# Kernel tuning notes

Hardware: AMD Instinct MI355X
Metric: run time of the kernel (lower is better)

The kernel has to match this reference:

```python
import jax, jax.numpy as jnp
import numpy as np

POSITIVE_MULT = 3.0  # init kwarg positive_mult
MIN_K = 10


def _ohem_single(pred, tgt):
    """OHEM MSE for one flattened sample. pred, tgt: [N]."""
    N = pred.shape[0]
    loss = (pred - tgt) ** 2  # elementwise MSE (reduction='none')
    pos = tgt > 0
    num_pos = jnp.sum(pos.astype(jnp.int32))
    # k = num_pos * positive_mult, clamped so k + num_pos <= N  =>  k = min(3p, N-p)
    k = jnp.minimum((num_pos.astype(jnp.float32) * POSITIVE_MULT).astype(jnp.int32),
                    N - num_pos)
    full_mean = jnp.mean(loss)
    # positive mean (safe denom; branch unused when num_pos small => k < 10)
    pos_mean = jnp.sum(jnp.where(pos, loss, 0.0)) / jnp.maximum(num_pos, 1).astype(loss.dtype)
    # top-k over negative losses: mask positives to -inf, sort descending,
    # take first k via index mask (k is traced, so no dynamic shapes)
    neg_loss = jnp.where(pos, -jnp.inf, loss)
    sorted_desc = -jnp.sort(-neg_loss)
    idx = jnp.arange(N)
    topk_mean = jnp.sum(jnp.where(idx < k, sorted_desc, 0.0)) / jnp.maximum(k, 1).astype(loss.dtype)
    ohem = pos_mean + topk_mean
    return jnp.where(k < MIN_K, full_mean, ohem)


def reference(x, char_target, aff_target):
    B, _, H, W = x.shape
    pred_r = x[:, 0].reshape(B, -1)  # region scores
    pred_a = x[:, 1].reshape(B, -1)  # affinity scores
    # bilinear resize, half-pixel centers == torch align_corners=False
    ct = jax.image.resize(char_target, (B, 1, H, W), method='bilinear').reshape(B, -1)
    at = jax.image.resize(aff_target, (B, 1, H, W), method='bilinear').reshape(B, -1)
    char_loss = jax.vmap(_ohem_single)(pred_r, ct)  # [B]
    aff_loss = jax.vmap(_ohem_single)(pred_a, at)   # [B]
    return jnp.mean(char_loss + aff_loss)


def setup_inputs() -> dict:
    key = jax.random.key(0)
    k1, k2, k3 = jax.random.split(key, 3)
    x = jax.random.normal(k1, (32, 2, 640, 640), dtype=jnp.float32)
    char_target = jax.random.normal(k2, (32, 1, 320, 320), dtype=jnp.float32)
    aff_target = jax.random.normal(k3, (32, 1, 320, 320), dtype=jnp.float32)
    return {"x": x, "char_target": char_target, "aff_target": aff_target}
```

## Files before the change

### kernel.cpp

```cpp
#include <hip/hip_runtime.h>

#define NS 64
#define HH 640
#define WW 640
#define NPIX (HH * WW)
#define TH 320
#define TW 320
#define MINK 10
#define BPS 40
#define TPB 320
#define ITERS 4

__device__ __forceinline__ float resize_scalar(const float* __restrict__ tgt, int y, int xc) {
    float sy = fmaxf(0.5f * (float)y - 0.25f, 0.0f);
    int y0 = (int)sy;
    float fy = sy - (float)y0;
    int y1 = min(y0 + 1, TH - 1);
    float sx = fmaxf(0.5f * (float)xc - 0.25f, 0.0f);
    int x0 = (int)sx;
    float fx = sx - (float)x0;
    int x1 = min(x0 + 1, TW - 1);
    const float* r0 = tgt + y0 * TW;
    const float* r1 = tgt + y1 * TW;
    float top = (1.0f - fx) * r0[x0] + fx * r0[x1];
    float bot = (1.0f - fx) * r1[x0] + fx * r1[x1];
    return (1.0f - fy) * top + fy * bot;
}

__global__ __launch_bounds__(TPB) void k_reduce(const float* __restrict__ x,
                                                const float* __restrict__ ct,
                                                const float* __restrict__ at,
                                                float* __restrict__ partA,
                                                float* __restrict__ partP,
                                                int* __restrict__ partC) {
    int bid = blockIdx.x;
    int s = bid / BPS, blk = bid % BPS;
    int b = s >> 1, c = s & 1;
    const float* pred = x + (size_t)s * NPIX;
    const float* tgt = (c == 0 ? ct : at) + (size_t)b * (TH * TW);

    int tid = threadIdx.x;
    int u = tid % 80;
    int rr = tid / 80;
    int rbase = blk * 16;

    float fy = (rr & 1) ? 0.25f : 0.75f;
    float gy = 1.0f - fy;
    int xq = 4 * u;
    int xl = max(xq - 1, 0);
    int xr = min(xq + 4, TW - 1);

    float sA = 0.0f, sP = 0.0f;
    int cP = 0;

#pragma unroll
    for (int i = 0; i < ITERS; ++i) {
        int y = rbase + rr + 4 * i;
        int y0raw = (y >> 1) + (y & 1) - 1;
        int y0 = max(y0raw, 0);
        int y1 = min(y0raw + 1, TH - 1);
        const float* r0 = tgt + y0 * TW;
        const float* r1 = tgt + y1 * TW;

        float4 a4 = *reinterpret_cast<const float4*>(r0 + xq);
        float La = r0[xl], Ra = r0[xr];
        float4 b4 = *reinterpret_cast<const float4*>(r1 + xq);
        float Lb = r1[xl], Rb = r1[xr];

        float mL = gy * La + fy * Lb;
        float m0 = gy * a4.x + fy * b4.x;
        float m1 = gy * a4.y + fy * b4.y;
        float m2 = gy * a4.z + fy * b4.z;
        float m3 = gy * a4.w + fy * b4.w;
        float mR = gy * Ra + fy * Rb;

        float tv[8];
        tv[0] = 0.25f * mL + 0.75f * m0;
        tv[1] = 0.75f * m0 + 0.25f * m1;
        tv[2] = 0.25f * m0 + 0.75f * m1;
        tv[3] = 0.75f * m1 + 0.25f * m2;
        tv[4] = 0.25f * m1 + 0.75f * m2;
        tv[5] = 0.75f * m2 + 0.25f * m3;
        tv[6] = 0.25f * m2 + 0.75f * m3;
        tv[7] = 0.75f * m3 + 0.25f * mR;

        const float* pr = pred + y * WW + 8 * u;
        float4 p0 = *reinterpret_cast<const float4*>(pr);
        float4 p1 = *reinterpret_cast<const float4*>(pr + 4);
        float pv[8] = {p0.x, p0.y, p0.z, p0.w, p1.x, p1.y, p1.z, p1.w};

#pragma unroll
        for (int j = 0; j < 8; ++j) {
            float d = pv[j] - tv[j];
            float l = d * d;
            sA += l;
            bool pos = tv[j] > 0.0f;
            sP += pos ? l : 0.0f;
            cP += pos ? 1 : 0;
        }
    }

    for (int off = 32; off > 0; off >>= 1) {
        sA += __shfl_down(sA, off);
        sP += __shfl_down(sP, off);
        cP += __shfl_down(cP, off);
    }
    __shared__ float shA[5], shP[5];
    __shared__ int shC[5];
    int w = tid >> 6;
    if ((tid & 63) == 0) { shA[w] = sA; shP[w] = sP; shC[w] = cP; }
    __syncthreads();
    if (tid == 0) {
        float a = 0.0f, p = 0.0f;
        int ci = 0;
        for (int q = 0; q < 5; ++q) { a += shA[q]; p += shP[q]; ci += shC[q]; }
        partA[s * BPS + blk] = a;
        partP[s * BPS + blk] = p;
        partC[s * BPS + blk] = ci;
    }
}

__global__ __launch_bounds__(256) void k_topk(const float* __restrict__ x,
                                              const float* __restrict__ ct,
                                              const float* __restrict__ at,
                                              const int* __restrict__ partC,
                                              float* __restrict__ topk) {
    int s = blockIdx.x;
    __shared__ int pSh;
    if (threadIdx.x < 64) {
        int v = (threadIdx.x < BPS) ? partC[s * BPS + threadIdx.x] : 0;
        for (int off = 32; off > 0; off >>= 1) v += __shfl_down(v, off);
        if (threadIdx.x == 0) pSh = v;
    }
    __syncthreads();
    int p = pSh;
    int k = min((int)((float)p * 3.0f), NPIX - p);
    if (k < MINK || k >= NPIX - p) return;

    int b = s >> 1, c = s & 1;
    const float* pred = x + (size_t)s * NPIX;
    const float* tgt = (c == 0 ? ct : at) + (size_t)b * (TH * TW);

    __shared__ unsigned int hcnt[2048];
    __shared__ float hsum[2048];
    __shared__ unsigned int selBin;
    __shared__ unsigned int remShared;
    __shared__ float sumTopShared;

    if (threadIdx.x == 0) { remShared = (unsigned int)k; sumTopShared = 0.0f; }

    const int shiftv[3] = {21, 10, 0};
    const unsigned int maskv[3] = {0x7FFu, 0x7FFu, 0x3FFu};
    unsigned int prefix = 0;

    for (int pass = 0; pass < 3; ++pass) {
        for (int i = threadIdx.x; i < 2048; i += 256) { hcnt[i] = 0u; hsum[i] = 0.0f; }
        __syncthreads();
        for (int e = threadIdx.x; e < NPIX; e += 256) {
            int yy = e / WW, xx = e % WW;
            float tv = resize_scalar(tgt, yy, xx);
            if (tv > 0.0f) continue;
            float d = pred[e] - tv;
            float l = d * d;
            unsigned int bits = __float_as_uint(l);
            bool match;
            if (pass == 0) match = true;
            else if (pass == 1) match = ((bits >> 21) == prefix);
            else match = ((bits >> 10) == prefix);
            if (match) {
                unsigned int bin = (bits >> shiftv[pass]) & maskv[pass];
                atomicAdd(&hcnt[bin], 1u);
                atomicAdd(&hsum[bin], l);
            }
        }
        __syncthreads();
        if (threadIdx.x == 0) {
            unsigned int remS = remShared;
            int nb = (int)maskv[pass] + 1;
            unsigned int cum = 0; float sAbove = 0.0f; unsigned int bsel = 0;
            for (int bin = nb - 1; bin >= 0; --bin) {
                unsigned int cc = hcnt[bin];
                if (cum + cc >= remS) { bsel = (unsigned int)bin; break; }
                cum += cc; sAbove += hsum[bin];
            }
            selBin = bsel;
            remShared = remS - cum;
            sumTopShared += sAbove;
        }
        __syncthreads();
        if (pass == 0) prefix = selBin;
        else if (pass == 1) prefix = (prefix << 11) | selBin;
        __syncthreads();
    }
    if (threadIdx.x == 0) {
        unsigned int bits = (prefix << 10) | selBin;
        float v = __uint_as_float(bits);
        topk[s] = sumTopShared + (float)remShared * v;
    }
}

__global__ void k_final(const float* __restrict__ partA, const float* __restrict__ partP,
                        const int* __restrict__ partC, const float* __restrict__ topk,
                        float* __restrict__ out) {
    int s = threadIdx.x;
    float a = 0.0f, pp = 0.0f;
    int p = 0;
    const float4* pa4 = reinterpret_cast<const float4*>(partA + s * BPS);
    const float4* pp4 = reinterpret_cast<const float4*>(partP + s * BPS);
    const int4*   pc4 = reinterpret_cast<const int4*>(partC + s * BPS);
#pragma unroll
    for (int q = 0; q < BPS / 4; ++q) {
        float4 va = pa4[q]; a += va.x + va.y + va.z + va.w;
        float4 vp = pp4[q]; pp += vp.x + vp.y + vp.z + vp.w;
        int4 vc = pc4[q]; p += vc.x + vc.y + vc.z + vc.w;
    }
    int k = min((int)((float)p * 3.0f), NPIX - p);
    float lossv;
    if (k < MINK) {
        lossv = a / (float)NPIX;
    } else {
        float nn = a - pp;
        float tsum = (k >= NPIX - p) ? nn : topk[s];
        lossv = pp / (float)max(p, 1) + tsum / (float)max(k, 1);
    }
    for (int off = 32; off > 0; off >>= 1) lossv += __shfl_down(lossv, off);
    if (s == 0) out[0] = lossv / 32.0f;
}

extern "C" void kernel_launch(void* const* d_in, const int* in_sizes, int n_in,
                              void* d_out, int out_size, void* d_ws, size_t ws_size,
                              hipStream_t stream) {
    const float* x  = (const float*)d_in[0];
    const float* ct = (const float*)d_in[1];
    const float* at = (const float*)d_in[2];
    float* out = (float*)d_out;

    float* partA = (float*)d_ws;
    float* partP = partA + NS * BPS;
    int*   partC = (int*)(partP + NS * BPS);
    float* topk  = (float*)(partC + NS * BPS);

    k_reduce<<<dim3(NS * BPS), dim3(TPB), 0, stream>>>(x, ct, at, partA, partP, partC);
    k_topk<<<dim3(NS), dim3(256), 0, stream>>>(x, ct, at, partC, topk);
    k_final<<<dim3(1), dim3(64), 0, stream>>>(partA, partP, partC, topk, out);
}
```

Measured before the change: 30.84 us.

## Fuse reduce, top-k and final kernels via last-block completion counters

Merges the three kernels into one launch: each block writes its partial sums, bumps a per-sample and then a global atomic counter, and the last block to finish performs the final combine and any needed top-k radix selection serially over samples. It also remaps block indices across 8 groups and transposes the partial-sum layout. This removes inter-kernel launch gaps and the separate top-k and final launches, at the cost of a memset and of running any top-k selection on a single workgroup, which would be slow if that path were ever taken.

```diff
diff --git a/kernel.cpp b/kernel.cpp
--- a/kernel.cpp
+++ b/kernel.cpp
@@ -10,6 +10,7 @@
 #define BPS 40
 #define TPB 320
 #define ITERS 4
+#define NWG (NS * BPS)
 
 __device__ __forceinline__ float resize_scalar(const float* __restrict__ tgt, int y, int xc) {
     float sy = fmaxf(0.5f * (float)y - 0.25f, 0.0f);
@@ -27,13 +28,17 @@
     return (1.0f - fy) * top + fy * bot;
 }
 
-__global__ __launch_bounds__(TPB) void k_reduce(const float* __restrict__ x,
-                                                const float* __restrict__ ct,
-                                                const float* __restrict__ at,
-                                                float* __restrict__ partA,
-                                                float* __restrict__ partP,
-                                                int* __restrict__ partC) {
-    int bid = blockIdx.x;
+__global__ __launch_bounds__(TPB) void k_fused(const float* __restrict__ x,
+                                               const float* __restrict__ ct,
+                                               const float* __restrict__ at,
+                                               float* __restrict__ partA,
+                                               float* __restrict__ partP,
+                                               int* __restrict__ partC,
+                                               int* __restrict__ cntS,
+                                               int* __restrict__ cntG,
+                                               float* __restrict__ out) {
+    int orig = blockIdx.x;
+    int bid = (orig & 7) * (NWG >> 3) + (orig >> 3);
     int s = bid / BPS, blk = bid % BPS;
     int b = s >> 1, c = s & 1;
     const float* pred = x + (size_t)s * NPIX;
@@ -110,121 +115,125 @@
     int w = tid >> 6;
     if ((tid & 63) == 0) { shA[w] = sA; shP[w] = sP; shC[w] = cP; }
     __syncthreads();
+
+    __shared__ int lastFlag;
     if (tid == 0) {
         float a = 0.0f, p = 0.0f;
         int ci = 0;
         for (int q = 0; q < 5; ++q) { a += shA[q]; p += shP[q]; ci += shC[q]; }
-        partA[s * BPS + blk] = a;
-        partP[s * BPS + blk] = p;
-        partC[s * BPS + blk] = ci;
-    }
-}
-
-__global__ __launch_bounds__(256) void k_topk(const float* __restrict__ x,
-                                              const float* __restrict__ ct,
-                                              const float* __restrict__ at,
-                                              const int* __restrict__ partC,
-                                              float* __restrict__ topk) {
-    int s = blockIdx.x;
-    __shared__ int pSh;
-    if (threadIdx.x < 64) {
-        int v = (threadIdx.x < BPS) ? partC[s * BPS + threadIdx.x] : 0;
-        for (int off = 32; off > 0; off >>= 1) v += __shfl_down(v, off);
-        if (threadIdx.x == 0) pSh = v;
-    }
-    __syncthreads();
-    int p = pSh;
-    int k = min((int)((float)p * 3.0f), NPIX - p);
-    if (k < MINK || k >= NPIX - p) return;
-
-    int b = s >> 1, c = s & 1;
-    const float* pred = x + (size_t)s * NPIX;
-    const float* tgt = (c == 0 ? ct : at) + (size_t)b * (TH * TW);
+        partA[blk * NS + s] = a;
+        partP[blk * NS + s] = p;
+        partC[blk * NS + s] = ci;
+        __threadfence();
+        int f = 0;
+        if (atomicAdd(&cntS[s], 1) == BPS - 1) {
+            __threadfence();
+            if (atomicAdd(cntG, 1) == NS - 1) f = 1;
+        }
+        lastFlag = f;
+    }
+    __syncthreads();
+    if (!lastFlag) return;
+
+    __threadfence();
+    __syncthreads();
+
+    __shared__ float lossSh[NS], topkSh[NS];
+    __shared__ int flagSh[NS], pSh[NS];
+    if (tid < NS) {
+        float a = 0.0f, pp = 0.0f;
+        int p = 0;
+        for (int q = 0; q < BPS; ++q) {
+            a  += partA[q * NS + tid];
+            pp += partP[q * NS + tid];
+            p  += partC[q * NS + tid];
+        }
+        int k = min((int)((float)p * 3.0f), NPIX - p);
+        pSh[tid] = p;
+        topkSh[tid] = 0.0f;
+        flagSh[tid] = (k >= MINK && k < NPIX - p) ? 1 : 0;
+        float lossv;
+        if (k < MINK) {
+            lossv = a / (float)NPIX;
+        } else {
+            float nn = a - pp;
+            float ts = (k >= NPIX - p) ? nn : 0.0f;
+            lossv = pp / (float)max(p, 1) + ts / (float)max(k, 1);
+        }
+        lossSh[tid] = lossv;
+    }
+    __syncthreads();
 
     __shared__ unsigned int hcnt[2048];
     __shared__ float hsum[2048];
-    __shared__ unsigned int selBin;
-    __shared__ unsigned int remShared;
-    __shared__ float sumTopShared;
-
-    if (threadIdx.x == 0) { remShared = (unsigned int)k; sumTopShared = 0.0f; }
-
-    const int shiftv[3] = {21, 10, 0};
-    const unsigned int maskv[3] = {0x7FFu, 0x7FFu, 0x3FFu};
-    unsigned int prefix = 0;
-
-    for (int pass = 0; pass < 3; ++pass) {
-        for (int i = threadIdx.x; i < 2048; i += 256) { hcnt[i] = 0u; hsum[i] = 0.0f; }
+    __shared__ unsigned int selBin, remSh;
+    __shared__ float sumTopSh;
+    for (int s2 = 0; s2 < NS; ++s2) {
+        if (!flagSh[s2]) continue;
+        int p2 = pSh[s2];
+        int k2 = min((int)((float)p2 * 3.0f), NPIX - p2);
+        const float* pred2 = x + (size_t)s2 * NPIX;
+        const float* tgt2 = ((s2 & 1) == 0 ? ct : at) + (size_t)(s2 >> 1) * (TH * TW);
+        if (tid == 0) { remSh = (unsigned int)k2; sumTopSh = 0.0f; }
+        const int shiftv[3] = {21, 10, 0};
+        const unsigned int maskv[3] = {0x7FFu, 0x7FFu, 0x3FFu};
+        unsigned int prefix = 0;
+        for (int pass = 0; pass < 3; ++pass) {
+            for (int i = tid; i < 2048; i += TPB) { hcnt[i] = 0u; hsum[i] = 0.0f; }
+            __syncthreads();
+            for (int e = tid; e < NPIX; e += TPB) {
+                int yy = e / WW, xx = e % WW;
+                float tv = resize_scalar(tgt2, yy, xx);
+                if (tv > 0.0f) continue;
+                float d = pred2[e] - tv;
+                float l = d * d;
+                unsigned int bits = __float_as_uint(l);
+                bool match;
+                if (pass == 0) match = true;
+                else if (pass == 1) match = ((bits >> 21) == prefix);
+                else match = ((bits >> 10) == prefix);
+                if (match) {
+                    unsigned int bin = (bits >> shiftv[pass]) & maskv[pass];
+                    atomicAdd(&hcnt[bin], 1u);
+                    atomicAdd(&hsum[bin], l);
+                }
+            }
+            __syncthreads();
+            if (tid == 0) {
+                unsigned int remS = remSh;
+                int nb = (int)maskv[pass] + 1;
+                unsigned int cum = 0; float sAb = 0.0f; unsigned int bsel = 0;
+                for (int bin = nb - 1; bin >= 0; --bin) {
+                    unsigned int cc = hcnt[bin];
+                    if (cum + cc >= remS) { bsel = (unsigned int)bin; break; }
+                    cum += cc; sAb += hsum[bin];
+                }
+                selBin = bsel;
+                remSh = remS - cum;
+                sumTopSh += sAb;
+            }
+            __syncthreads();
+            if (pass == 0) prefix = selBin;
+            else if (pass == 1) prefix = (prefix << 11) | selBin;
+            __syncthreads();
+        }
+        if (tid == 0) {
+            unsigned int bits = (prefix << 10) | selBin;
+            topkSh[s2] = sumTopSh + (float)remSh * __uint_as_float(bits);
+        }
         __syncthreads();
-        for (int e = threadIdx.x; e < NPIX; e += 256) {
-            int yy = e / WW, xx = e % WW;
-            float tv = resize_scalar(tgt, yy, xx);
-            if (tv > 0.0f) continue;
-            float d = pred[e] - tv;
-            float l = d * d;
-            unsigned int bits = __float_as_uint(l);
-            bool match;
-            if (pass == 0) match = true;
-            else if (pass == 1) match = ((bits >> 21) == prefix);
-            else match = ((bits >> 10) == prefix);
-            if (match) {
-                unsigned int bin = (bits >> shiftv[pass]) & maskv[pass];
-                atomicAdd(&hcnt[bin], 1u);
-                atomicAdd(&hsum[bin], l);
-            }
-        }
-        __syncthreads();
-        if (threadIdx.x == 0) {
-            unsigned int remS = remShared;
-            int nb = (int)maskv[pass] + 1;
-            unsigned int cum = 0; float sAbove = 0.0f; unsigned int bsel = 0;
-            for (int bin = nb - 1; bin >= 0; --bin) {
-                unsigned int cc = hcnt[bin];
-                if (cum + cc >= remS) { bsel = (unsigned int)bin; break; }
-                cum += cc; sAbove += hsum[bin];
-            }
-            selBin = bsel;
-            remShared = remS - cum;
-            sumTopShared += sAbove;
-        }
-        __syncthreads();
-        if (pass == 0) prefix = selBin;
-        else if (pass == 1) prefix = (prefix << 11) | selBin;
-        __syncthreads();
-    }
-    if (threadIdx.x == 0) {
-        unsigned int bits = (prefix << 10) | selBin;
-        float v = __uint_as_float(bits);
-        topk[s] = sumTopShared + (float)remShared * v;
-    }
-}
-
-__global__ void k_final(const float* __restrict__ partA, const float* __restrict__ partP,
-                        const int* __restrict__ partC, const float* __restrict__ topk,
-                        float* __restrict__ out) {
-    int s = threadIdx.x;
-    float a = 0.0f, pp = 0.0f;
-    int p = 0;
-    const float4* pa4 = reinterpret_cast<const float4*>(partA + s * BPS);
-    const float4* pp4 = reinterpret_cast<const float4*>(partP + s * BPS);
-    const int4*   pc4 = reinterpret_cast<const int4*>(partC + s * BPS);
-#pragma unroll
-    for (int q = 0; q < BPS / 4; ++q) {
-        float4 va = pa4[q]; a += va.x + va.y + va.z + va.w;
-        float4 vp = pp4[q]; pp += vp.x + vp.y + vp.z + vp.w;
-        int4 vc = pc4[q]; p += vc.x + vc.y + vc.z + vc.w;
-    }
-    int k = min((int)((float)p * 3.0f), NPIX - p);
-    float lossv;
-    if (k < MINK) {
-        lossv = a / (float)NPIX;
-    } else {
-        float nn = a - pp;
-        float tsum = (k >= NPIX - p) ? nn : topk[s];
-        lossv = pp / (float)max(p, 1) + tsum / (float)max(k, 1);
-    }
-    for (int off = 32; off > 0; off >>= 1) lossv += __shfl_down(lossv, off);
-    if (s == 0) out[0] = lossv / 32.0f;
+    }
+
+    if (tid < NS) {
+        float lossv = lossSh[tid];
+        if (flagSh[tid]) {
+            int p = pSh[tid];
+            int k = min((int)((float)p * 3.0f), NPIX - p);
+            lossv += topkSh[tid] / (float)max(k, 1);
+        }
+        for (int off = 32; off > 0; off >>= 1) lossv += __shfl_down(lossv, off);
+        if (tid == 0) out[0] = lossv / 32.0f;
+    }
 }
 
 extern "C" void kernel_launch(void* const* d_in, const int* in_sizes, int n_in,
@@ -236,11 +245,13 @@
     float* out = (float*)d_out;
 
     float* partA = (float*)d_ws;
-    float* partP = partA + NS * BPS;
-    int*   partC = (int*)(partP + NS * BPS);
-    float* topk  = (float*)(partC + NS * BPS);
-
-    k_reduce<<<dim3(NS * BPS), dim3(TPB), 0, stream>>>(x, ct, at, partA, partP, partC);
-    k_topk<<<dim3(NS), dim3(256), 0, stream>>>(x, ct, at, partC, topk);
-    k_final<<<dim3(1), dim3(64), 0, stream>>>(partA, partP, partC, topk, out);
+    float* partP = partA + NWG;
+    int*   partC = (int*)(partP + NWG);
+    int*   cntS  = partC + NWG;
+    int*   cntG  = cntS + NS;
+
+    hipMemsetAsync(cntS, 0, (NS + 1) * sizeof(int), stream);
+
+    k_fused<<<dim3(NWG), dim3(TPB), 0, stream>>>(x, ct, at, partA, partP, partC,
+                                                 cntS, cntG, out);
 }
```

After: 122.2 us. 296% more time.
